# Optimization experiments

Hardware: AMD Instinct MI355X
Metric: run time of the kernel (lower is better)

The kernel has to match this reference:

```python
import jax, jax.numpy as jnp
import numpy as np

V, D, B, S, T, MAXLEN = 32000, 256, 4, 512, 256, 512


def _gru(x, Wih, Whh, bih, bhh):
    """torch-style GRU over x:[B,L,Din] -> [B,L,D]. Weight rows ordered [r,z,n]."""
    Dh = Whh.shape[1]
    xW = x @ Wih.T + bih  # [B,L,3D] precompute input projections

    def step(h, xw):
        hW = h @ Whh.T + bhh
        xr, xz, xn = jnp.split(xw, 3, axis=-1)
        hr, hz, hn = jnp.split(hW, 3, axis=-1)
        r = jax.nn.sigmoid(xr + hr)
        z = jax.nn.sigmoid(xz + hz)
        n = jnp.tanh(xn + r * hn)
        h = (1.0 - z) * n + z * h
        return h, h

    h0 = jnp.zeros((x.shape[0], Dh), x.dtype)
    _, ys = jax.lax.scan(step, h0, jnp.swapaxes(xW, 0, 1))
    return jnp.swapaxes(ys, 0, 1)


def setup_inputs() -> dict:
    key = jax.random.key(0)
    ks = jax.random.split(key, 24)

    def n(k, shape, scale=0.02):
        return (jax.random.normal(k, shape, jnp.float32) * scale).astype(jnp.float32)

    inp = {
        "src": jax.random.randint(ks[0], (B, S), 0, V),
        "tgt": jax.random.randint(ks[1], (B, T), 0, V),
        "emb": n(ks[2], (V, D)),
        "pos": n(ks[3], (MAXLEN, D)),
        # encoder forward direction
        "ef_wih": n(ks[4], (3 * D, D)), "ef_whh": n(ks[5], (3 * D, D)),
        "ef_bih": n(ks[6], (3 * D,)), "ef_bhh": n(ks[7], (3 * D,)),
        # encoder backward direction
        "eb_wih": n(ks[8], (3 * D, D)), "eb_whh": n(ks[9], (3 * D, D)),
        "eb_bih": n(ks[10], (3 * D,)), "eb_bhh": n(ks[11], (3 * D,)),
        # decoder
        "d_wih": n(ks[12], (3 * D, D)), "d_whh": n(ks[13], (3 * D, D)),
        "d_bih": n(ks[14], (3 * D,)), "d_bhh": n(ks[15], (3 * D,)),
        "Wq": n(ks[16], (D, D)),
        "Wk": n(ks[17], (D, 2 * D)),
        "Wgen": n(ks[18], (V, 3 * D)), "bgen": n(ks[19], (V,)),
        "Wgate": n(ks[20], (1, 3 * D)), "bgate": n(ks[21], (1,)),
    }
    return inp


def reference(src, tgt, emb, pos,
              ef_wih, ef_whh, ef_bih, ef_bhh,
              eb_wih, eb_whh, eb_bih, eb_bhh,
              d_wih, d_whh, d_bih, d_bhh,
              Wq, Wk, Wgen, bgen, Wgate, bgate):
    b, s = src.shape
    t = tgt.shape[1]
    d = emb.shape[1]
    v = emb.shape[0]

    src_emb = emb[src] + pos[:s][None]          # [B,S,D]
    enc_f = _gru(src_emb, ef_wih, ef_whh, ef_bih, ef_bhh)
    enc_b = _gru(src_emb[:, ::-1], eb_wih, eb_whh, eb_bih, eb_bhh)[:, ::-1]
    enc_out = jnp.concatenate([enc_f, enc_b], axis=-1)  # [B,S,2D]

    tgt_emb = emb[tgt] + pos[:t][None]
    dec_out = _gru(tgt_emb, d_wih, d_whh, d_bih, d_bhh)  # [B,T,D]

    Q = dec_out @ Wq.T                           # [B,T,D]
    K = enc_out @ Wk.T                           # [B,S,D]
    scores = jnp.einsum('btd,bsd->bts', Q, K) / jnp.sqrt(jnp.asarray(d, jnp.float32))
    pos_probs = jax.nn.softmax(scores, axis=-1)  # [B,T,S]

    # copy distribution: scatter attention mass into vocab buckets (== one_hot bmm)
    P_copy = jnp.zeros((b, t, v), pos_probs.dtype).at[
        jnp.arange(b)[:, None, None],
        jnp.arange(t)[None, :, None],
        src[:, None, :],
    ].add(pos_probs)

    ctx_f = jnp.einsum('bts,bsd->btd', pos_probs, enc_f)
    ctx_b = jnp.einsum('bts,bsd->btd', pos_probs, enc_b)
    combined = jnp.concatenate([dec_out, ctx_f, ctx_b], axis=-1)  # [B,T,3D]

    P_gen = jax.nn.softmax(combined @ Wgen.T + bgen, axis=-1)     # [B,T,V]
    gate = jax.nn.sigmoid(combined @ Wgate.T + bgate)             # [B,T,1]
    return gate * P_gen + (1.0 - gate) * P_copy
```

## Files before the change

kernel.cpp:

```cpp
#include <hip/hip_runtime.h>
#include <hip/hip_bf16.h>
#include <math.h>

#define VV   32000
#define DIM  256
#define BB   4
#define SS   512
#define TT   256
#define D2   512
#define D3   768

typedef __attribute__((ext_vector_type(8))) short s16x8;
typedef __attribute__((ext_vector_type(4))) float f32x4;

__device__ __forceinline__ float rcp_(float x) { return __builtin_amdgcn_rcpf(x); }
__device__ __forceinline__ float sigmoidf_(float x) { return rcp_(1.0f + __expf(-x)); }
__device__ __forceinline__ float tanhf_(float x) {
    float t = __expf(-2.0f * x);
    return (1.0f - t) * rcp_(1.0f + t);
}
__device__ __forceinline__ short f2bf(float f) {
    unsigned u = __float_as_uint(f);
    u += 0x7FFFu + ((u >> 16) & 1u);
    return (short)(u >> 16);
}

#define BAR_LGKM() asm volatile("s_waitcnt lgkmcnt(0)\n\ts_barrier" ::: "memory")

struct PDesc {
    const int* tok;
    const float* Wt;
    const float* bias;
    float* C;
    int M;
    int lmask;
};

__global__ __launch_bounds__(512) void k_proj(const float* __restrict__ emb,
                                              const float* __restrict__ pos,
                                              PDesc p0, PDesc p1, PDesc p2) {
    PDesc p = (blockIdx.z == 0) ? p0 : ((blockIdx.z == 1) ? p1 : p2);
    int brow = blockIdx.y * 256;
    if (brow >= p.M) return;
    int bcol = blockIdx.x * 128;

    __shared__ __align__(16) short As[256 * 32];
    __shared__ __align__(16) short Bs[128 * 32];
    int tid = threadIdx.x;
    int lane = tid & 63, wv = tid >> 6;
    int wm = wv >> 1, wn = wv & 1;
    const int ll = lane & 15, lh = lane >> 4;

    f32x4 acc[4][4];
#pragma unroll
    for (int i = 0; i < 4; i++)
#pragma unroll
        for (int j = 0; j < 4; j++) acc[i][j] = (f32x4){0.f, 0.f, 0.f, 0.f};

    const int ar = tid >> 1, ak = (tid & 1) * 16;
    const int br = tid >> 2, bk = (tid & 3) * 8;
    const int grow = brow + ar;
    const float* erow = emb + (size_t)p.tok[grow] * DIM;
    const float* prow = pos + (size_t)(grow & p.lmask) * DIM;

    for (int k0 = 0; k0 < DIM; k0 += 32) {
        float4 a0 = *(const float4*)(erow + k0 + ak);
        float4 a1 = *(const float4*)(erow + k0 + ak + 4);
        float4 a2 = *(const float4*)(erow + k0 + ak + 8);
        float4 a3 = *(const float4*)(erow + k0 + ak + 12);
        float4 q0 = *(const float4*)(prow + k0 + ak);
        float4 q1 = *(const float4*)(prow + k0 + ak + 4);
        float4 q2 = *(const float4*)(prow + k0 + ak + 8);
        float4 q3 = *(const float4*)(prow + k0 + ak + 12);
        const float* bp = &p.Wt[(size_t)(bcol + br) * DIM + k0 + bk];
        float4 b0 = *(const float4*)bp;
        float4 b1 = *(const float4*)(bp + 4);
        s16x8 va0, va1, vb;
        va0[0] = f2bf(a0.x + q0.x); va0[1] = f2bf(a0.y + q0.y);
        va0[2] = f2bf(a0.z + q0.z); va0[3] = f2bf(a0.w + q0.w);
        va0[4] = f2bf(a1.x + q1.x); va0[5] = f2bf(a1.y + q1.y);
        va0[6] = f2bf(a1.z + q1.z); va0[7] = f2bf(a1.w + q1.w);
        va1[0] = f2bf(a2.x + q2.x); va1[1] = f2bf(a2.y + q2.y);
        va1[2] = f2bf(a2.z + q2.z); va1[3] = f2bf(a2.w + q2.w);
        va1[4] = f2bf(a3.x + q3.x); va1[5] = f2bf(a3.y + q3.y);
        va1[6] = f2bf(a3.z + q3.z); va1[7] = f2bf(a3.w + q3.w);
        vb[0] = f2bf(b0.x); vb[1] = f2bf(b0.y); vb[2] = f2bf(b0.z); vb[3] = f2bf(b0.w);
        vb[4] = f2bf(b1.x); vb[5] = f2bf(b1.y); vb[6] = f2bf(b1.z); vb[7] = f2bf(b1.w);

        __syncthreads();
        *(s16x8*)&As[ar * 32 + ak] = va0;
        *(s16x8*)&As[ar * 32 + ak + 8] = va1;
        *(s16x8*)&Bs[br * 32 + bk] = vb;
        __syncthreads();

        s16x8 af[4], bf[4];
#pragma unroll
        for (int mt = 0; mt < 4; ++mt)
            af[mt] = *(const s16x8*)&As[(wm * 64 + mt * 16 + ll) * 32 + lh * 8];
#pragma unroll
        for (int nt = 0; nt < 4; ++nt)
            bf[nt] = *(const s16x8*)&Bs[(wn * 64 + nt * 16 + ll) * 32 + lh * 8];
#pragma unroll
        for (int mt = 0; mt < 4; ++mt)
#pragma unroll
            for (int nt = 0; nt < 4; ++nt)
                acc[mt][nt] = __builtin_amdgcn_mfma_f32_16x16x32_bf16(af[mt], bf[nt], acc[mt][nt], 0, 0, 0);
    }

#pragma unroll
    for (int mt = 0; mt < 4; ++mt) {
        int row = brow + wm * 64 + mt * 16 + lh * 4;
#pragma unroll
        for (int nt = 0; nt < 4; ++nt) {
            int col = bcol + wn * 64 + nt * 16 + ll;
            float bv = p.bias[col];
#pragma unroll
            for (int q = 0; q < 4; ++q)
                p.C[(size_t)(row + q) * D3 + col] = acc[mt][nt][q] + bv;
        }
    }
}

struct GDesc {
    const float* A; int lda;
    const float* Bt; int ldb;
    const float* bias;
    float* C; int ldc;
    int M, N;
};

#define BMM 128
#define BNN 128
#define BKK 8

__global__ __launch_bounds__(256) void k_gemmb(GDesc d0, GDesc d1, GDesc d2) {
    GDesc d = (blockIdx.z == 0) ? d0 : ((blockIdx.z == 1) ? d1 : d2);
    int brow = blockIdx.y * BMM, bcol = blockIdx.x * BNN;
    if (brow >= d.M || bcol >= d.N) return;

    __shared__ float As[BKK][BMM + 4];
    __shared__ float Bs[BKK][BNN + 4];
    const int K = d.lda;
    int tid = threadIdx.x;
    int tx = tid & 15, ty = tid >> 4;
    float acc[8][8];
#pragma unroll
    for (int i = 0; i < 8; i++)
#pragma unroll
        for (int j = 0; j < 8; j++) acc[i][j] = 0.0f;

    int lr = tid >> 1;
    int lk = (tid & 1) * 4;
    for (int k0 = 0; k0 < K; k0 += BKK) {
        float4 a4 = *(const float4*)&d.A[(size_t)(brow + lr) * d.lda + k0 + lk];
        float4 b4 = *(const float4*)&d.Bt[(size_t)(bcol + lr) * d.ldb + k0 + lk];
        As[lk + 0][lr] = a4.x; As[lk + 1][lr] = a4.y; As[lk + 2][lr] = a4.z; As[lk + 3][lr] = a4.w;
        Bs[lk + 0][lr] = b4.x; Bs[lk + 1][lr] = b4.y; Bs[lk + 2][lr] = b4.z; Bs[lk + 3][lr] = b4.w;
        __syncthreads();
#pragma unroll
        for (int kk = 0; kk < BKK; kk++) {
            float4 a0 = *(const float4*)&As[kk][ty * 8];
            float4 a1 = *(const float4*)&As[kk][ty * 8 + 4];
            float4 b0 = *(const float4*)&Bs[kk][tx * 8];
            float4 b1 = *(const float4*)&Bs[kk][tx * 8 + 4];
            float av[8] = {a0.x, a0.y, a0.z, a0.w, a1.x, a1.y, a1.z, a1.w};
            float bv[8] = {b0.x, b0.y, b0.z, b0.w, b1.x, b1.y, b1.z, b1.w};
#pragma unroll
            for (int i = 0; i < 8; i++)
#pragma unroll
                for (int j = 0; j < 8; j++) acc[i][j] += av[i] * bv[j];
        }
        __syncthreads();
    }

#pragma unroll
    for (int i = 0; i < 8; i++) {
        size_t row = brow + ty * 8 + i;
        float4 c0 = make_float4(acc[i][0], acc[i][1], acc[i][2], acc[i][3]);
        float4 c1 = make_float4(acc[i][4], acc[i][5], acc[i][6], acc[i][7]);
        *(float4*)&d.C[row * d.ldc + bcol + tx * 8] = c0;
        *(float4*)&d.C[row * d.ldc + bcol + tx * 8 + 4] = c1;
    }
}

#define HSTRIDE 576
#define HBUF    (4 * HSTRIDE)
#define NCVT8   ((size_t)VV * D3 / 8)

__global__ __launch_bounds__(1024) void k_gru(const float* __restrict__ ef_x,
                                              const float* __restrict__ eb_x,
                                              const float* __restrict__ d_x,
                                              const float* __restrict__ ef_whh, const float* __restrict__ ef_bhh,
                                              const float* __restrict__ eb_whh, const float* __restrict__ eb_bhh,
                                              const float* __restrict__ d_whh, const float* __restrict__ d_bhh,
                                              float* __restrict__ enc_out,
                                              float* __restrict__ dec_out,
                                              const float* __restrict__ wgen,
                                              short* __restrict__ wgen_bf,
                                              float* __restrict__ rowsum,
                                              int do_cvt) {
    int tid = threadIdx.x;
    int bid = blockIdx.x;

    if (bid >= 3) {
        int cb = bid - 3;
        if (cb == 0) rowsum[tid] = 0.0f;
        if (do_cvt) {
            size_t i = (size_t)cb * 1024 + tid;
            if (i < NCVT8) {
                const float4* p = (const float4*)(wgen + i * 8);
                float4 a = p[0], b4 = p[1];
                s16x8 v;
                v[0] = f2bf(a.x); v[1] = f2bf(a.y); v[2] = f2bf(a.z); v[3] = f2bf(a.w);
                v[4] = f2bf(b4.x); v[5] = f2bf(b4.y); v[6] = f2bf(b4.z); v[7] = f2bf(b4.w);
                *(s16x8*)(wgen_bf + i * 8) = v;
            }
        }
        return;
    }

    __shared__ __align__(16) char hb[2 * HBUF];
    int dir = bid;
    const float *xw, *Whh, *bhh;
    int L;
    if (dir == 0)      { xw = ef_x; Whh = ef_whh; bhh = ef_bhh; L = SS; }
    else if (dir == 1) { xw = eb_x; Whh = eb_whh; bhh = eb_bhh; L = SS; }
    else               { xw = d_x;  Whh = d_whh;  bhh = d_bhh;  L = TT; }

    const int wv = tid >> 6;
    const int lane = tid & 63;
    const int jj = lane & 15;
    const int hi = lane >> 4;
    const int b = hi;

    if (tid < 288) {
        f32x4 z = {0.f, 0.f, 0.f, 0.f};
        *(f32x4*)(hb + tid * 16) = z;
    }

    s16x8 wf[3][8];
#pragma unroll
    for (int g = 0; g < 3; ++g) {
        const int nrow = g * 256 + wv * 16 + jj;
        const float* wp = Whh + (size_t)nrow * 256 + hi * 8;
#pragma unroll
        for (int sk = 0; sk < 8; ++sk) {
            float4 w0 = *(const float4*)(wp + sk * 32);
            float4 w1 = *(const float4*)(wp + sk * 32 + 4);
            s16x8 v;
            v[0] = f2bf(w0.x); v[1] = f2bf(w0.y); v[2] = f2bf(w0.z); v[3] = f2bf(w0.w);
            v[4] = f2bf(w1.x); v[5] = f2bf(w1.y); v[6] = f2bf(w1.z); v[7] = f2bf(w1.w);
            wf[g][sk] = v;
        }
    }

    const int j0 = wv * 16 + jj;
    const float br0 = bhh[j0], bz0 = bhh[256 + j0], bn0 = bhh[512 + j0];

    const int arow = jj >> 2;
    const int abase = arow * HSTRIDE + hi * 16;
    const int wo0 = b * HSTRIDE + 2 * j0;

    const int s0 = (dir == 1) ? (L - 1) : 0;
    const int sst = (dir == 1) ? -1 : 1;
    const float* xq = xw + ((size_t)b * L + s0) * D3 + j0;
    float* op;
    int ostride;
    if (dir == 2) { op = dec_out + ((size_t)b * TT + s0) * DIM + j0; ostride = sst * DIM; }
    else          { op = enc_out + ((size_t)b * SS + s0) * D2 + (dir == 1 ? DIM : 0) + j0; ostride = sst * D2; }
    const int xstride = sst * D3;

    float c0 = xq[0], c1 = xq[256], c2 = xq[512];

    float h0 = 0.f;
    int cur = 0;
    __syncthreads();

    for (int st = 0; st < L; ++st) {
        xq += xstride;
        float n0 = xq[0], n1 = xq[256], n2 = xq[512];

        const char* hcur = hb + cur * HBUF;
        f32x4 a00 = {0.f, 0.f, 0.f, 0.f}, a10 = a00, a20 = a00;
#pragma unroll
        for (int sk = 0; sk < 8; ++sk) {
            s16x8 af = *(const s16x8*)(hcur + abase + 64 * sk);
            a00 = __builtin_amdgcn_mfma_f32_16x16x32_bf16(af, wf[0][sk], a00, 0, 0, 0);
            a10 = __builtin_amdgcn_mfma_f32_16x16x32_bf16(af, wf[1][sk], a10, 0, 0, 0);
            a20 = __builtin_amdgcn_mfma_f32_16x16x32_bf16(af, wf[2][sk], a20, 0, 0, 0);
        }

        float r0 = sigmoidf_(c0 + a00[0] + br0);
        float z0 = sigmoidf_(c1 + a10[0] + bz0);
        float nn0 = tanhf_(c2 + r0 * (a20[0] + bn0));
        h0 = (1.f - z0) * nn0 + z0 * h0;

        char* hnxt = hb + (cur ^ 1) * HBUF;
        *(short*)(hnxt + wo0) = f2bf(h0);
        op[0] = h0;
        BAR_LGKM();

        cur ^= 1;
        c0 = n0; c1 = n1; c2 = n2;
        op += ostride;
    }
}

__global__ __launch_bounds__(512) void k_attn(const float* __restrict__ Qb,
                                              const float* __restrict__ Kb,
                                              const float* __restrict__ enc_out,
                                              const float* __restrict__ dec_out,
                                              const float* __restrict__ Wgate,
                                              const float* __restrict__ bgate,
                                              float* __restrict__ probs,
                                              short* __restrict__ cmb,
                                              float* __restrict__ gate) {
    __shared__ float q[DIM];
    __shared__ float sc[SS];
    __shared__ float red[512];
    __shared__ float par[2][2][DIM];
    int row = blockIdx.x;
    int b = row >> 8;
    int tid = threadIdx.x;

    if (tid < DIM) q[tid] = Qb[(size_t)row * DIM + tid];
    __syncthreads();

    const float scale = 0.0625f;
    {
        const float* kr = Kb + ((size_t)b * SS + tid) * DIM;
        float acc = 0.0f;
        for (int k = 0; k < DIM; k += 4) {
            float4 k4 = *(const float4*)&kr[k];
            acc += k4.x * q[k] + k4.y * q[k + 1] + k4.z * q[k + 2] + k4.w * q[k + 3];
        }
        sc[tid] = acc * scale;
    }
    __syncthreads();

    red[tid] = sc[tid];
    __syncthreads();
    for (int o = 256; o > 0; o >>= 1) {
        if (tid < o) red[tid] = fmaxf(red[tid], red[tid + o]);
        __syncthreads();
    }
    float m = red[0];
    __syncthreads();

    float e0 = __expf(sc[tid] - m);
    sc[tid] = e0;
    red[tid] = e0;
    __syncthreads();
    for (int o = 256; o > 0; o >>= 1) {
        if (tid < o) red[tid] += red[tid + o];
        __syncthreads();
    }
    float inv = rcp_(red[0]);
    __syncthreads();

    sc[tid] *= inv;
    probs[(size_t)row * SS + tid] = sc[tid];
    __syncthreads();

    {
        int d = tid & 255, sh = tid >> 8;
        float accf = 0.0f, accb = 0.0f;
        const float* ep = enc_out + ((size_t)b * SS + sh * 256) * D2 + d;
        const float* pp = &sc[sh * 256];
        for (int s = 0; s < 256; s++) {
            float p = pp[s];
            accf += p * ep[(size_t)s * D2];
            accb += p * ep[(size_t)s * D2 + DIM];
        }
        par[sh][0][d] = accf;
        par[sh][1][d] = accb;
    }
    __syncthreads();

    if (tid < DIM) {
        float af = par[0][0][tid] + par[1][0][tid];
        float ab = par[0][1][tid] + par[1][1][tid];
        float dv = dec_out[(size_t)row * DIM + tid];
        cmb[(size_t)row * D3 + tid] = f2bf(dv);
        cmb[(size_t)row * D3 + DIM + tid] = f2bf(af);
        cmb[(size_t)row * D3 + 2 * DIM + tid] = f2bf(ab);
        red[tid] = dv * Wgate[tid] + af * Wgate[DIM + tid] + ab * Wgate[2 * DIM + tid];
    }
    __syncthreads();
    for (int o = 128; o > 0; o >>= 1) {
        if (tid < o) red[tid] += red[tid + o];
        __syncthreads();
    }
    if (tid == 0) gate[row] = sigmoidf_(red[0] + bgate[0]);
}

__global__ __launch_bounds__(512) void k_gen_bf(const short* __restrict__ A,
                                                const short* __restrict__ Bbf,
                                                const float* __restrict__ bias,
                                                float* __restrict__ C,
                                                float* __restrict__ rowsum) {
    __shared__ __align__(16) short As[256 * 32];
    __shared__ __align__(16) short Bs[128 * 32];
    int tid = threadIdx.x;
    int lane = tid & 63, wv = tid >> 6;
    int wm = wv >> 1, wn = wv & 1;
    int brow = blockIdx.y * 256, bcol = blockIdx.x * 128;
    f32x4 acc[4][4];
#pragma unroll
    for (int i = 0; i < 4; i++)
#pragma unroll
        for (int j = 0; j < 4; j++) acc[i][j] = (f32x4){0.f, 0.f, 0.f, 0.f};

    const int ca0 = tid, ca1 = tid + 512, cb = tid;
    const int ll = lane & 15, lh = lane >> 4;

    for (int k0 = 0; k0 < D3; k0 += 32) {
        s16x8 va0 = *(const s16x8*)&A[(size_t)(brow + (ca0 >> 2)) * D3 + k0 + (ca0 & 3) * 8];
        s16x8 va1 = *(const s16x8*)&A[(size_t)(brow + (ca1 >> 2)) * D3 + k0 + (ca1 & 3) * 8];
        s16x8 vb  = *(const s16x8*)&Bbf[(size_t)(bcol + (cb >> 2)) * D3 + k0 + (cb & 3) * 8];

        __syncthreads();
        *(s16x8*)&As[ca0 * 8] = va0;
        *(s16x8*)&As[ca1 * 8] = va1;
        *(s16x8*)&Bs[cb * 8] = vb;
        __syncthreads();

        s16x8 af[4], bf[4];
#pragma unroll
        for (int mt = 0; mt < 4; ++mt)
            af[mt] = *(const s16x8*)&As[(wm * 64 + mt * 16 + ll) * 32 + lh * 8];
#pragma unroll
        for (int nt = 0; nt < 4; ++nt)
            bf[nt] = *(const s16x8*)&Bs[(wn * 64 + nt * 16 + ll) * 32 + lh * 8];
#pragma unroll
        for (int mt = 0; mt < 4; ++mt)
#pragma unroll
            for (int nt = 0; nt < 4; ++nt)
                acc[mt][nt] = __builtin_amdgcn_mfma_f32_16x16x32_bf16(af[mt], bf[nt], acc[mt][nt], 0, 0, 0);
    }

#pragma unroll
    for (int nt = 0; nt < 4; ++nt) {
        float bv = bias[bcol + wn * 64 + nt * 16 + ll];
#pragma unroll
        for (int mt = 0; mt < 4; ++mt)
#pragma unroll
            for (int q = 0; q < 4; ++q) acc[mt][nt][q] += bv;
    }

#pragma unroll
    for (int mt = 0; mt < 4; ++mt) {
        int row = brow + wm * 64 + mt * 16 + lh * 4;
#pragma unroll
        for (int nt = 0; nt < 4; ++nt) {
            int col = bcol + wn * 64 + nt * 16 + ll;
#pragma unroll
            for (int q = 0; q < 4; ++q)
                C[(size_t)(row + q) * VV + col] = acc[mt][nt][q];
        }
    }

#pragma unroll
    for (int mt = 0; mt < 4; ++mt) {
#pragma unroll
        for (int q = 0; q < 4; ++q) {
            float se = __expf(acc[mt][0][q]) + __expf(acc[mt][1][q]) +
                       __expf(acc[mt][2][q]) + __expf(acc[mt][3][q]);
#pragma unroll
            for (int off = 1; off < 16; off <<= 1)
                se += __shfl_xor(se, off);
            if (ll == 0) {
                int row = brow + wm * 64 + mt * 16 + lh * 4 + q;
                atomicAdd(&rowsum[row], se);
            }
        }
    }
}

__global__ __launch_bounds__(512) void k_gen(const short* __restrict__ A,
                                             const float* __restrict__ Bw,
                                             const float* __restrict__ bias,
                                             float* __restrict__ C,
                                             float* __restrict__ rowsum) {
    __shared__ __align__(16) short As[256 * 32];
    __shared__ __align__(16) short Bs[128 * 32];
    int tid = threadIdx.x;
    int lane = tid & 63, wv = tid >> 6;
    int wm = wv >> 1, wn = wv & 1;
    int brow = blockIdx.y * 256, bcol = blockIdx.x * 128;
    f32x4 acc[4][4];
#pragma unroll
    for (int i = 0; i < 4; i++)
#pragma unroll
        for (int j = 0; j < 4; j++) acc[i][j] = (f32x4){0.f, 0.f, 0.f, 0.f};

    const int ca0 = tid, ca1 = tid + 512, cb = tid;
    const int ll = lane & 15, lh = lane >> 4;

    for (int k0 = 0; k0 < D3; k0 += 32) {
        s16x8 va0 = *(const s16x8*)&A[(size_t)(brow + (ca0 >> 2)) * D3 + k0 + (ca0 & 3) * 8];
        s16x8 va1 = *(const s16x8*)&A[(size_t)(brow + (ca1 >> 2)) * D3 + k0 + (ca1 & 3) * 8];
        const float* bp = &Bw[(size_t)(bcol + (cb >> 2)) * D3 + k0 + (cb & 3) * 8];
        float4 b0 = *(const float4*)bp;
        float4 b1 = *(const float4*)(bp + 4);
        s16x8 vb;
        vb[0] = f2bf(b0.x); vb[1] = f2bf(b0.y); vb[2] = f2bf(b0.z); vb[3] = f2bf(b0.w);
        vb[4] = f2bf(b1.x); vb[5] = f2bf(b1.y); vb[6] = f2bf(b1.z); vb[7] = f2bf(b1.w);

        __syncthreads();
        *(s16x8*)&As[ca0 * 8] = va0;
        *(s16x8*)&As[ca1 * 8] = va1;
        *(s16x8*)&Bs[cb * 8] = vb;
        __syncthreads();

        s16x8 af[4], bf[4];
#pragma unroll
        for (int mt = 0; mt < 4; ++mt)
            af[mt] = *(const s16x8*)&As[(wm * 64 + mt * 16 + ll) * 32 + lh * 8];
#pragma unroll
        for (int nt = 0; nt < 4; ++nt)
            bf[nt] = *(const s16x8*)&Bs[(wn * 64 + nt * 16 + ll) * 32 + lh * 8];
#pragma unroll
        for (int mt = 0; mt < 4; ++mt)
#pragma unroll
            for (int nt = 0; nt < 4; ++nt)
                acc[mt][nt] = __builtin_amdgcn_mfma_f32_16x16x32_bf16(af[mt], bf[nt], acc[mt][nt], 0, 0, 0);
    }

#pragma unroll
    for (int nt = 0; nt < 4; ++nt) {
        float bv = bias[bcol + wn * 64 + nt * 16 + ll];
#pragma unroll
        for (int mt = 0; mt < 4; ++mt)
#pragma unroll
            for (int q = 0; q < 4; ++q) acc[mt][nt][q] += bv;
    }

#pragma unroll
    for (int mt = 0; mt < 4; ++mt) {
        int row = brow + wm * 64 + mt * 16 + lh * 4;
#pragma unroll
        for (int nt = 0; nt < 4; ++nt) {
            int col = bcol + wn * 64 + nt * 16 + ll;
#pragma unroll
            for (int q = 0; q < 4; ++q)
                C[(size_t)(row + q) * VV + col] = acc[mt][nt][q];
        }
    }

#pragma unroll
    for (int mt = 0; mt < 4; ++mt) {
#pragma unroll
        for (int q = 0; q < 4; ++q) {
            float se = __expf(acc[mt][0][q]) + __expf(acc[mt][1][q]) +
                       __expf(acc[mt][2][q]) + __expf(acc[mt][3][q]);
#pragma unroll
            for (int off = 1; off < 16; off <<= 1)
                se += __shfl_xor(se, off);
            if (ll == 0) {
                int row = brow + wm * 64 + mt * 16 + lh * 4 + q;
                atomicAdd(&rowsum[row], se);
            }
        }
    }
}

__global__ __launch_bounds__(256) void k_finsc(const int* __restrict__ src,
                                               const float* __restrict__ probs,
                                               const float* __restrict__ gate,
                                               const float* __restrict__ rowsum,
                                               float* __restrict__ out) {
    int row = blockIdx.x;
    int b = row >> 8;
    int tid = threadIdx.x;
    float g = gate[row];
    float inv = g / rowsum[row];
    float* op = out + (size_t)row * VV;

    for (int i = tid; i < VV / 4; i += 256) {
        float4 l = *(const float4*)&op[i * 4];
        l.x = __expf(l.x) * inv;
        l.y = __expf(l.y) * inv;
        l.z = __expf(l.z) * inv;
        l.w = __expf(l.w) * inv;
        *(float4*)&op[i * 4] = l;
    }
    __syncthreads();

    float og = 1.0f - g;
#pragma unroll
    for (int h = 0; h < 2; ++h) {
        int s = tid + h * 256;
        float val = og * probs[(size_t)row * SS + s];
        atomicAdd(&op[src[b * SS + s]], val);
    }
}

extern "C" void kernel_launch(void* const* d_in, const int* in_sizes, int n_in,
                              void* d_out, int out_size, void* d_ws, size_t ws_size,
                              hipStream_t stream) {
    const int*   src    = (const int*)d_in[0];
    const int*   tgt    = (const int*)d_in[1];
    const float* emb    = (const float*)d_in[2];
    const float* pos    = (const float*)d_in[3];
    const float* ef_wih = (const float*)d_in[4];
    const float* ef_whh = (const float*)d_in[5];
    const float* ef_bih = (const float*)d_in[6];
    const float* ef_bhh = (const float*)d_in[7];
    const float* eb_wih = (const float*)d_in[8];
    const float* eb_whh = (const float*)d_in[9];
    const float* eb_bih = (const float*)d_in[10];
    const float* eb_bhh = (const float*)d_in[11];
    const float* d_wih  = (const float*)d_in[12];
    const float* d_whh  = (const float*)d_in[13];
    const float* d_bih  = (const float*)d_in[14];
    const float* d_bhh  = (const float*)d_in[15];
    const float* Wq     = (const float*)d_in[16];
    const float* Wk     = (const float*)d_in[17];
    const float* Wgen   = (const float*)d_in[18];
    const float* bgen   = (const float*)d_in[19];
    const float* Wgate  = (const float*)d_in[20];
    const float* bgate  = (const float*)d_in[21];
    float* out = (float*)d_out;
    float* ws  = (float*)d_ws;

    float* ef_x     = ws;
    float* eb_x     = ef_x + (size_t)BB * SS * D3;
    float* d_x      = eb_x + (size_t)BB * SS * D3;
    float* enc_out  = d_x + (size_t)BB * TT * D3;
    float* dec_out  = enc_out + (size_t)BB * SS * D2;
    float* Qb       = dec_out + (size_t)BB * TT * DIM;
    float* Kb       = Qb + (size_t)BB * TT * DIM;
    float* probs    = Kb + (size_t)BB * SS * DIM;
    short* cmb_bf   = (short*)(probs + (size_t)BB * TT * SS);
    float* gate     = (float*)(cmb_bf + (size_t)BB * TT * D3);
    float* rowsum   = gate + 1024;
    short* wgen_bf  = (short*)(rowsum + 1024);
    const bool use_bf = ws_size >= (size_t)((char*)(wgen_bf + (size_t)VV * D3) - (char*)d_ws);

    {
        PDesc e0 = {src, ef_wih, ef_bih, ef_x, BB * SS, SS - 1};
        PDesc e1 = {src, eb_wih, eb_bih, eb_x, BB * SS, SS - 1};
        PDesc e2 = {tgt, d_wih, d_bih, d_x, BB * TT, TT - 1};
        k_proj<<<dim3(D3 / 128, BB * SS / 256, 3), 512, 0, stream>>>(emb, pos, e0, e1, e2);
    }

    {
        int ncvtb = (int)((NCVT8 + 1023) / 1024);
        k_gru<<<3 + ncvtb, 1024, 0, stream>>>(ef_x, eb_x, d_x,
                                              ef_whh, ef_bhh, eb_whh, eb_bhh, d_whh, d_bhh,
                                              enc_out, dec_out,
                                              Wgen, wgen_bf, rowsum, use_bf ? 1 : 0);
    }

    {
        GDesc q0 = {dec_out, DIM, Wq, DIM, nullptr, Qb, DIM, BB * TT, DIM};
        GDesc q1 = {enc_out, D2, Wk, D2, nullptr, Kb, DIM, BB * SS, DIM};
        k_gemmb<<<dim3(DIM / BNN, BB * SS / BMM, 2), 256, 0, stream>>>(q0, q1, q1);
    }

    k_attn<<<BB * TT, 512, 0, stream>>>(Qb, Kb, enc_out, dec_out, Wgate, bgate,
                                        probs, cmb_bf, gate);

    if (use_bf)
        k_gen_bf<<<dim3(VV / 128, (BB * TT) / 256), 512, 0, stream>>>(cmb_bf, wgen_bf, bgen, out, rowsum);
    else
        k_gen<<<dim3(VV / 128, (BB * TT) / 256), 512, 0, stream>>>(cmb_bf, Wgen, bgen, out, rowsum);

    k_finsc<<<BB * TT, 256, 0, stream>>>(src, probs, gate, rowsum, out);
}
```

Baseline: 1.072 ms.

## Rework GRU to 512 threads, MFMA Q/K projection, bf16 logits intermediate

The GRU kernel now runs 512 threads per block, with each wave computing two 16-column slices. The gate math switches to exact-division sigmoid and tanh. The fp32 FMA GEMM for the Q/K projections is replaced with a bf16 MFMA tile kernel. When the workspace is large enough, generator logits are stored as bf16 in a separate buffer and expanded by a new finisher kernel, which halves the intermediate logit traffic at the cost of logit precision. Exact division may lengthen the serial recurrence step.

```diff
diff --git a/kernel.cpp b/kernel.cpp
--- a/kernel.cpp
+++ b/kernel.cpp
@@ -15,14 +15,18 @@
 
 __device__ __forceinline__ float rcp_(float x) { return __builtin_amdgcn_rcpf(x); }
 __device__ __forceinline__ float sigmoidf_(float x) { return rcp_(1.0f + __expf(-x)); }
-__device__ __forceinline__ float tanhf_(float x) {
-    float t = __expf(-2.0f * x);
-    return (1.0f - t) * rcp_(1.0f + t);
+__device__ __forceinline__ float sigmoid_p(float x) { return 1.0f / (1.0f + __expf(-x)); }
+__device__ __forceinline__ float tanh_p(float x) {
+    float e2 = __expf(2.0f * x);
+    return (e2 - 1.0f) / (e2 + 1.0f);
 }
 __device__ __forceinline__ short f2bf(float f) {
     unsigned u = __float_as_uint(f);
     u += 0x7FFFu + ((u >> 16) & 1u);
     return (short)(u >> 16);
+}
+__device__ __forceinline__ float bf2f(short s) {
+    return __uint_as_float(((unsigned)(unsigned short)s) << 16);
 }
 
 #define BAR_LGKM() asm volatile("s_waitcnt lgkmcnt(0)\n\ts_barrier" ::: "memory")
@@ -121,65 +125,83 @@
     }
 }
 
-struct GDesc {
-    const float* A; int lda;
-    const float* Bt; int ldb;
-    const float* bias;
-    float* C; int ldc;
-    int M, N;
+struct QDesc {
+    const float* A; int K;
+    const float* Bt;
+    float* C;
+    int M;
 };
 
-#define BMM 128
-#define BNN 128
-#define BKK 8
-
-__global__ __launch_bounds__(256) void k_gemmb(GDesc d0, GDesc d1, GDesc d2) {
-    GDesc d = (blockIdx.z == 0) ? d0 : ((blockIdx.z == 1) ? d1 : d2);
-    int brow = blockIdx.y * BMM, bcol = blockIdx.x * BNN;
-    if (brow >= d.M || bcol >= d.N) return;
-
-    __shared__ float As[BKK][BMM + 4];
-    __shared__ float Bs[BKK][BNN + 4];
-    const int K = d.lda;
+__global__ __launch_bounds__(512) void k_qk(QDesc q0d, QDesc q1d) {
+    QDesc p = (blockIdx.z == 0) ? q0d : q1d;
+    int brow = blockIdx.y * 256;
+    if (brow >= p.M) return;
+    int bcol = blockIdx.x * 128;
+    const int K = p.K;
+
+    __shared__ __align__(16) short As[256 * 32];
+    __shared__ __align__(16) short Bs[128 * 32];
     int tid = threadIdx.x;
-    int tx = tid & 15, ty = tid >> 4;
-    float acc[8][8];
-#pragma unroll
-    for (int i = 0; i < 8; i++)
-#pragma unroll
-        for (int j = 0; j < 8; j++) acc[i][j] = 0.0f;
-
-    int lr = tid >> 1;
-    int lk = (tid & 1) * 4;
-    for (int k0 = 0; k0 < K; k0 += BKK) {
-        float4 a4 = *(const float4*)&d.A[(size_t)(brow + lr) * d.lda + k0 + lk];
-        float4 b4 = *(const float4*)&d.Bt[(size_t)(bcol + lr) * d.ldb + k0 + lk];
-        As[lk + 0][lr] = a4.x; As[lk + 1][lr] = a4.y; As[lk + 2][lr] = a4.z; As[lk + 3][lr] = a4.w;
-        Bs[lk + 0][lr] = b4.x; Bs[lk + 1][lr] = b4.y; Bs[lk + 2][lr] = b4.z; Bs[lk + 3][lr] = b4.w;
+    int lane = tid & 63, wv = tid >> 6;
+    int wm = wv >> 1, wn = wv & 1;
+    const int ll = lane & 15, lh = lane >> 4;
+
+    f32x4 acc[4][4];
+#pragma unroll
+    for (int i = 0; i < 4; i++)
+#pragma unroll
+        for (int j = 0; j < 4; j++) acc[i][j] = (f32x4){0.f, 0.f, 0.f, 0.f};
+
+    const int ar = tid >> 1, ak = (tid & 1) * 16;
+    const int br = tid >> 2, bk = (tid & 3) * 8;
+
+    for (int k0 = 0; k0 < K; k0 += 32) {
+        const float* ap = &p.A[(size_t)(brow + ar) * K + k0 + ak];
+        float4 a0 = *(const float4*)ap;
+        float4 a1 = *(const float4*)(ap + 4);
+        float4 a2 = *(const float4*)(ap + 8);
+        float4 a3 = *(const float4*)(ap + 12);
+        const float* bp = &p.Bt[(size_t)(bcol + br) * K + k0 + bk];
+        float4 b0 = *(const float4*)bp;
+        float4 b1 = *(const float4*)(bp + 4);
+        s16x8 va0, va1, vb;
+        va0[0] = f2bf(a0.x); va0[1] = f2bf(a0.y); va0[2] = f2bf(a0.z); va0[3] = f2bf(a0.w);
+        va0[4] = f2bf(a1.x); va0[5] = f2bf(a1.y); va0[6] = f2bf(a1.z); va0[7] = f2bf(a1.w);
+        va1[0] = f2bf(a2.x); va1[1] = f2bf(a2.y); va1[2] = f2bf(a2.z); va1[3] = f2bf(a2.w);
+        va1[4] = f2bf(a3.x); va1[5] = f2bf(a3.y); va1[6] = f2bf(a3.z); va1[7] = f2bf(a3.w);
+        vb[0] = f2bf(b0.x); vb[1] = f2bf(b0.y); vb[2] = f2bf(b0.z); vb[3] = f2bf(b0.w);
+        vb[4] = f2bf(b1.x); vb[5] = f2bf(b1.y); vb[6] = f2bf(b1.z); vb[7] = f2bf(b1.w);
+
         __syncthreads();
-#pragma unroll
-        for (int kk = 0; kk < BKK; kk++) {
-            float4 a0 = *(const float4*)&As[kk][ty * 8];
-            float4 a1 = *(const float4*)&As[kk][ty * 8 + 4];
-            float4 b0 = *(const float4*)&Bs[kk][tx * 8];
-            float4 b1 = *(const float4*)&Bs[kk][tx * 8 + 4];
-            float av[8] = {a0.x, a0.y, a0.z, a0.w, a1.x, a1.y, a1.z, a1.w};
-            float bv[8] = {b0.x, b0.y, b0.z, b0.w, b1.x, b1.y, b1.z, b1.w};
-#pragma unroll
-            for (int i = 0; i < 8; i++)
-#pragma unroll
-                for (int j = 0; j < 8; j++) acc[i][j] += av[i] * bv[j];
-        }
+        *(s16x8*)&As[ar * 32 + ak] = va0;
+        *(s16x8*)&As[ar * 32 + ak + 8] = va1;
+        *(s16x8*)&Bs[br * 32 + bk] = vb;
         __syncthreads();
-    }
-
-#pragma unroll
-    for (int i = 0; i < 8; i++) {
-        size_t row = brow + ty * 8 + i;
-        float4 c0 = make_float4(acc[i][0], acc[i][1], acc[i][2], acc[i][3]);
-        float4 c1 = make_float4(acc[i][4], acc[i][5], acc[i][6], acc[i][7]);
-        *(float4*)&d.C[row * d.ldc + bcol + tx * 8] = c0;
-        *(float4*)&d.C[row * d.ldc + bcol + tx * 8 + 4] = c1;
+
+        s16x8 af[4], bf[4];
+#pragma unroll
+        for (int mt = 0; mt < 4; ++mt)
+            af[mt] = *(const s16x8*)&As[(wm * 64 + mt * 16 + ll) * 32 + lh * 8];
+#pragma unroll
+        for (int nt = 0; nt < 4; ++nt)
+            bf[nt] = *(const s16x8*)&Bs[(wn * 64 + nt * 16 + ll) * 32 + lh * 8];
+#pragma unroll
+        for (int mt = 0; mt < 4; ++mt)
+#pragma unroll
+            for (int nt = 0; nt < 4; ++nt)
+                acc[mt][nt] = __builtin_amdgcn_mfma_f32_16x16x32_bf16(af[mt], bf[nt], acc[mt][nt], 0, 0, 0);
+    }
+
+#pragma unroll
+    for (int mt = 0; mt < 4; ++mt) {
+        int row = brow + wm * 64 + mt * 16 + lh * 4;
+#pragma unroll
+        for (int nt = 0; nt < 4; ++nt) {
+            int col = bcol + wn * 64 + nt * 16 + ll;
+#pragma unroll
+            for (int q = 0; q < 4; ++q)
+                p.C[(size_t)(row + q) * DIM + col] = acc[mt][nt][q];
+        }
     }
 }
 
@@ -187,26 +209,26 @@
 #define HBUF    (4 * HSTRIDE)
 #define NCVT8   ((size_t)VV * D3 / 8)
 
-__global__ __launch_bounds__(1024) void k_gru(const float* __restrict__ ef_x,
-                                              const float* __restrict__ eb_x,
-                                              const float* __restrict__ d_x,
-                                              const float* __restrict__ ef_whh, const float* __restrict__ ef_bhh,
-                                              const float* __restrict__ eb_whh, const float* __restrict__ eb_bhh,
-                                              const float* __restrict__ d_whh, const float* __restrict__ d_bhh,
-                                              float* __restrict__ enc_out,
-                                              float* __restrict__ dec_out,
-                                              const float* __restrict__ wgen,
-                                              short* __restrict__ wgen_bf,
-                                              float* __restrict__ rowsum,
-                                              int do_cvt) {
+__global__ __launch_bounds__(512, 2) void k_gru(const float* __restrict__ ef_x,
+                                                const float* __restrict__ eb_x,
+                                                const float* __restrict__ d_x,
+                                                const float* __restrict__ ef_whh, const float* __restrict__ ef_bhh,
+                                                const float* __restrict__ eb_whh, const float* __restrict__ eb_bhh,
+                                                const float* __restrict__ d_whh, const float* __restrict__ d_bhh,
+                                                float* __restrict__ enc_out,
+                                                float* __restrict__ dec_out,
+                                                const float* __restrict__ wgen,
+                                                short* __restrict__ wgen_bf,
+                                                float* __restrict__ rowsum,
+                                                int do_cvt) {
     int tid = threadIdx.x;
     int bid = blockIdx.x;
 
     if (bid >= 3) {
         int cb = bid - 3;
-        if (cb == 0) rowsum[tid] = 0.0f;
+        if (cb == 0) { rowsum[tid] = 0.0f; rowsum[tid + 512] = 0.0f; }
         if (do_cvt) {
-            size_t i = (size_t)cb * 1024 + tid;
+            size_t i = (size_t)cb * 512 + tid;
             if (i < NCVT8) {
                 const float4* p = (const float4*)(wgen + i * 8);
                 float4 a = p[0], b4 = p[1];
@@ -238,28 +260,32 @@
         *(f32x4*)(hb + tid * 16) = z;
     }
 
-    s16x8 wf[3][8];
-#pragma unroll
-    for (int g = 0; g < 3; ++g) {
-        const int nrow = g * 256 + wv * 16 + jj;
-        const float* wp = Whh + (size_t)nrow * 256 + hi * 8;
-#pragma unroll
-        for (int sk = 0; sk < 8; ++sk) {
-            float4 w0 = *(const float4*)(wp + sk * 32);
-            float4 w1 = *(const float4*)(wp + sk * 32 + 4);
-            s16x8 v;
-            v[0] = f2bf(w0.x); v[1] = f2bf(w0.y); v[2] = f2bf(w0.z); v[3] = f2bf(w0.w);
-            v[4] = f2bf(w1.x); v[5] = f2bf(w1.y); v[6] = f2bf(w1.z); v[7] = f2bf(w1.w);
-            wf[g][sk] = v;
-        }
-    }
-
-    const int j0 = wv * 16 + jj;
+    s16x8 wf[3][2][8];
+#pragma unroll
+    for (int g = 0; g < 3; ++g)
+#pragma unroll
+        for (int t = 0; t < 2; ++t) {
+            const int nrow = g * 256 + wv * 32 + t * 16 + jj;
+            const float* wp = Whh + (size_t)nrow * 256 + hi * 8;
+#pragma unroll
+            for (int sk = 0; sk < 8; ++sk) {
+                float4 w0 = *(const float4*)(wp + sk * 32);
+                float4 w1 = *(const float4*)(wp + sk * 32 + 4);
+                s16x8 v;
+                v[0] = f2bf(w0.x); v[1] = f2bf(w0.y); v[2] = f2bf(w0.z); v[3] = f2bf(w0.w);
+                v[4] = f2bf(w1.x); v[5] = f2bf(w1.y); v[6] = f2bf(w1.z); v[7] = f2bf(w1.w);
+                wf[g][t][sk] = v;
+            }
+        }
+
+    const int j0 = wv * 32 + jj, j1 = j0 + 16;
     const float br0 = bhh[j0], bz0 = bhh[256 + j0], bn0 = bhh[512 + j0];
+    const float br1 = bhh[j1], bz1 = bhh[256 + j1], bn1 = bhh[512 + j1];
 
     const int arow = jj >> 2;
     const int abase = arow * HSTRIDE + hi * 16;
     const int wo0 = b * HSTRIDE + 2 * j0;
+    const int wo1 = b * HSTRIDE + 2 * j1;
 
     const int s0 = (dir == 1) ? (L - 1) : 0;
     const int sst = (dir == 1) ? -1 : 1;
@@ -270,38 +296,47 @@
     else          { op = enc_out + ((size_t)b * SS + s0) * D2 + (dir == 1 ? DIM : 0) + j0; ostride = sst * D2; }
     const int xstride = sst * D3;
 
-    float c0 = xq[0], c1 = xq[256], c2 = xq[512];
-
-    float h0 = 0.f;
+    float c0 = xq[0], c1 = xq[256], c2 = xq[512], c3 = xq[16], c4 = xq[272], c5 = xq[528];
+
+    float h0 = 0.f, h1 = 0.f;
     int cur = 0;
     __syncthreads();
 
     for (int st = 0; st < L; ++st) {
         xq += xstride;
-        float n0 = xq[0], n1 = xq[256], n2 = xq[512];
+        float n0 = xq[0], n1 = xq[256], n2 = xq[512], n3 = xq[16], n4 = xq[272], n5 = xq[528];
 
         const char* hcur = hb + cur * HBUF;
-        f32x4 a00 = {0.f, 0.f, 0.f, 0.f}, a10 = a00, a20 = a00;
+        f32x4 a00 = {0.f, 0.f, 0.f, 0.f}, a01 = a00, a10 = a00, a11 = a00, a20 = a00, a21 = a00;
 #pragma unroll
         for (int sk = 0; sk < 8; ++sk) {
             s16x8 af = *(const s16x8*)(hcur + abase + 64 * sk);
-            a00 = __builtin_amdgcn_mfma_f32_16x16x32_bf16(af, wf[0][sk], a00, 0, 0, 0);
-            a10 = __builtin_amdgcn_mfma_f32_16x16x32_bf16(af, wf[1][sk], a10, 0, 0, 0);
-            a20 = __builtin_amdgcn_mfma_f32_16x16x32_bf16(af, wf[2][sk], a20, 0, 0, 0);
-        }
-
-        float r0 = sigmoidf_(c0 + a00[0] + br0);
-        float z0 = sigmoidf_(c1 + a10[0] + bz0);
-        float nn0 = tanhf_(c2 + r0 * (a20[0] + bn0));
+            a00 = __builtin_amdgcn_mfma_f32_16x16x32_bf16(af, wf[0][0][sk], a00, 0, 0, 0);
+            a01 = __builtin_amdgcn_mfma_f32_16x16x32_bf16(af, wf[0][1][sk], a01, 0, 0, 0);
+            a10 = __builtin_amdgcn_mfma_f32_16x16x32_bf16(af, wf[1][0][sk], a10, 0, 0, 0);
+            a11 = __builtin_amdgcn_mfma_f32_16x16x32_bf16(af, wf[1][1][sk], a11, 0, 0, 0);
+            a20 = __builtin_amdgcn_mfma_f32_16x16x32_bf16(af, wf[2][0][sk], a20, 0, 0, 0);
+            a21 = __builtin_amdgcn_mfma_f32_16x16x32_bf16(af, wf[2][1][sk], a21, 0, 0, 0);
+        }
+
+        float r0 = sigmoid_p(c0 + a00[0] + br0);
+        float z0 = sigmoid_p(c1 + a10[0] + bz0);
+        float nn0 = tanh_p(c2 + r0 * (a20[0] + bn0));
         h0 = (1.f - z0) * nn0 + z0 * h0;
+        float r1 = sigmoid_p(c3 + a01[0] + br1);
+        float z1 = sigmoid_p(c4 + a11[0] + bz1);
+        float nn1 = tanh_p(c5 + r1 * (a21[0] + bn1));
+        h1 = (1.f - z1) * nn1 + z1 * h1;
 
         char* hnxt = hb + (cur ^ 1) * HBUF;
         *(short*)(hnxt + wo0) = f2bf(h0);
+        *(short*)(hnxt + wo1) = f2bf(h1);
         op[0] = h0;
+        op[16] = h1;
         BAR_LGKM();
 
         cur ^= 1;
-        c0 = n0; c1 = n1; c2 = n2;
+        c0 = n0; c1 = n1; c2 = n2; c3 = n3; c4 = n4; c5 = n5;
         op += ostride;
     }
 }
@@ -394,51 +429,94 @@
     if (tid == 0) gate[row] = sigmoidf_(red[0] + bgate[0]);
 }
 
+#define GEN_PROLOGUE()                                                      \
+    __shared__ __align__(16) short As[256 * 32];                            \
+    __shared__ __align__(16) short Bs[128 * 32];                            \
+    int tid = threadIdx.x;                                                  \
+    int lane = tid & 63, wv = tid >> 6;                                     \
+    int wm = wv >> 1, wn = wv & 1;                                          \
+    int brow = blockIdx.y * 256, bcol = blockIdx.x * 128;                   \
+    f32x4 acc[4][4];                                                        \
+    _Pragma("unroll") for (int i = 0; i < 4; i++)                           \
+        _Pragma("unroll") for (int j = 0; j < 4; j++)                       \
+            acc[i][j] = (f32x4){0.f, 0.f, 0.f, 0.f};                        \
+    const int ca0 = tid, ca1 = tid + 512, cb = tid;                         \
+    const int ll = lane & 15, lh = lane >> 4;
+
+#define GEN_MAINLOOP(LOAD_B)                                                \
+    for (int k0 = 0; k0 < D3; k0 += 32) {                                   \
+        s16x8 va0 = *(const s16x8*)&A[(size_t)(brow + (ca0 >> 2)) * D3 + k0 + (ca0 & 3) * 8]; \
+        s16x8 va1 = *(const s16x8*)&A[(size_t)(brow + (ca1 >> 2)) * D3 + k0 + (ca1 & 3) * 8]; \
+        s16x8 vb; LOAD_B;                                                   \
+        __syncthreads();                                                    \
+        *(s16x8*)&As[ca0 * 8] = va0;                                        \
+        *(s16x8*)&As[ca1 * 8] = va1;                                        \
+        *(s16x8*)&Bs[cb * 8] = vb;                                          \
+        __syncthreads();                                                    \
+        s16x8 af[4], bf[4];                                                 \
+        _Pragma("unroll") for (int mt = 0; mt < 4; ++mt)                    \
+            af[mt] = *(const s16x8*)&As[(wm * 64 + mt * 16 + ll) * 32 + lh * 8]; \
+        _Pragma("unroll") for (int nt = 0; nt < 4; ++nt)                    \
+            bf[nt] = *(const s16x8*)&Bs[(wn * 64 + nt * 16 + ll) * 32 + lh * 8]; \
+        _Pragma("unroll") for (int mt = 0; mt < 4; ++mt)                    \
+            _Pragma("unroll") for (int nt = 0; nt < 4; ++nt)                \
+                acc[mt][nt] = __builtin_amdgcn_mfma_f32_16x16x32_bf16(af[mt], bf[nt], acc[mt][nt], 0, 0, 0); \
+    }
+
+#define LOADB_BF  vb = *(const s16x8*)&Bbf[(size_t)(bcol + (cb >> 2)) * D3 + k0 + (cb & 3) * 8]
+#define LOADB_F32 do {                                                      \
+        const float* bp = &Bw[(size_t)(bcol + (cb >> 2)) * D3 + k0 + (cb & 3) * 8]; \
+        float4 b0 = *(const float4*)bp; float4 b1 = *(const float4*)(bp + 4); \
+        vb[0] = f2bf(b0.x); vb[1] = f2bf(b0.y); vb[2] = f2bf(b0.z); vb[3] = f2bf(b0.w); \
+        vb[4] = f2bf(b1.x); vb[5] = f2bf(b1.y); vb[6] = f2bf(b1.z); vb[7] = f2bf(b1.w); } while (0)
+
+#define GEN_ROWSUM(EXPR)                                                    \
+    _Pragma("unroll") for (int mt = 0; mt < 4; ++mt)                        \
+        _Pragma("unroll") for (int q = 0; q < 4; ++q) {                     \
+            float se = (EXPR);                                              \
+            _Pragma("unroll") for (int off = 1; off < 16; off <<= 1)        \
+                se += __shfl_xor(se, off);                                  \
+            if (ll == 0) atomicAdd(&rowsum[brow + wm * 64 + mt * 16 + lh * 4 + q], se); \
+        }
+
+__global__ __launch_bounds__(512) void k_genb(const short* __restrict__ A,
+                                              const short* __restrict__ Bbf,
+                                              const float* __restrict__ bias,
+                                              short* __restrict__ C16,
+                                              float* __restrict__ rowsum) {
+    GEN_PROLOGUE();
+    GEN_MAINLOOP(LOADB_BF);
+    short lr[4][4][4];
+#pragma unroll
+    for (int nt = 0; nt < 4; ++nt) {
+        float bv = bias[bcol + wn * 64 + nt * 16 + ll];
+#pragma unroll
+        for (int mt = 0; mt < 4; ++mt)
+#pragma unroll
+            for (int q = 0; q < 4; ++q) lr[mt][nt][q] = f2bf(acc[mt][nt][q] + bv);
+    }
+#pragma unroll
+    for (int mt = 0; mt < 4; ++mt) {
+        int row = brow + wm * 64 + mt * 16 + lh * 4;
+#pragma unroll
+        for (int nt = 0; nt < 4; ++nt) {
+            int col = bcol + wn * 64 + nt * 16 + ll;
+#pragma unroll
+            for (int q = 0; q < 4; ++q)
+                C16[(size_t)(row + q) * VV + col] = lr[mt][nt][q];
+        }
+    }
+    GEN_ROWSUM(__expf(bf2f(lr[mt][0][q])) + __expf(bf2f(lr[mt][1][q])) +
+               __expf(bf2f(lr[mt][2][q])) + __expf(bf2f(lr[mt][3][q])));
+}
+
 __global__ __launch_bounds__(512) void k_gen_bf(const short* __restrict__ A,
                                                 const short* __restrict__ Bbf,
                                                 const float* __restrict__ bias,
                                                 float* __restrict__ C,
                                                 float* __restrict__ rowsum) {
-    __shared__ __align__(16) short As[256 * 32];
-    __shared__ __align__(16) short Bs[128 * 32];
-    int tid = threadIdx.x;
-    int lane = tid & 63, wv = tid >> 6;
-    int wm = wv >> 1, wn = wv & 1;
-    int brow = blockIdx.y * 256, bcol = blockIdx.x * 128;
-    f32x4 acc[4][4];
-#pragma unroll
-    for (int i = 0; i < 4; i++)
-#pragma unroll
-        for (int j = 0; j < 4; j++) acc[i][j] = (f32x4){0.f, 0.f, 0.f, 0.f};
-
-    const int ca0 = tid, ca1 = tid + 512, cb = tid;
-    const int ll = lane & 15, lh = lane >> 4;
-
-    for (int k0 = 0; k0 < D3; k0 += 32) {
-        s16x8 va0 = *(const s16x8*)&A[(size_t)(brow + (ca0 >> 2)) * D3 + k0 + (ca0 & 3) * 8];
-        s16x8 va1 = *(const s16x8*)&A[(size_t)(brow + (ca1 >> 2)) * D3 + k0 + (ca1 & 3) * 8];
-        s16x8 vb  = *(const s16x8*)&Bbf[(size_t)(bcol + (cb >> 2)) * D3 + k0 + (cb & 3) * 8];
-
-        __syncthreads();
-        *(s16x8*)&As[ca0 * 8] = va0;
-        *(s16x8*)&As[ca1 * 8] = va1;
-        *(s16x8*)&Bs[cb * 8] = vb;
-        __syncthreads();
-
-        s16x8 af[4], bf[4];
-#pragma unroll
-        for (int mt = 0; mt < 4; ++mt)
-            af[mt] = *(const s16x8*)&As[(wm * 64 + mt * 16 + ll) * 32 + lh * 8];
-#pragma unroll
-        for (int nt = 0; nt < 4; ++nt)
-            bf[nt] = *(const s16x8*)&Bs[(wn * 64 + nt * 16 + ll) * 32 + lh * 8];
-#pragma unroll
-        for (int mt = 0; mt < 4; ++mt)
-#pragma unroll
-            for (int nt = 0; nt < 4; ++nt)
-                acc[mt][nt] = __builtin_amdgcn_mfma_f32_16x16x32_bf16(af[mt], bf[nt], acc[mt][nt], 0, 0, 0);
-    }
-
+    GEN_PROLOGUE();
+    GEN_MAINLOOP(LOADB_BF);
 #pragma unroll
     for (int nt = 0; nt < 4; ++nt) {
         float bv = bias[bcol + wn * 64 + nt * 16 + ll];
@@ -447,7 +525,6 @@
 #pragma unroll
             for (int q = 0; q < 4; ++q) acc[mt][nt][q] += bv;
     }
-
 #pragma unroll
     for (int mt = 0; mt < 4; ++mt) {
         int row = brow + wm * 64 + mt * 16 + lh * 4;
@@ -459,22 +536,8 @@
                 C[(size_t)(row + q) * VV + col] = acc[mt][nt][q];
         }
     }
-
-#pragma unroll
-    for (int mt = 0; mt < 4; ++mt) {
-#pragma unroll
-        for (int q = 0; q < 4; ++q) {
-            float se = __expf(acc[mt][0][q]) + __expf(acc[mt][1][q]) +
-                       __expf(acc[mt][2][q]) + __expf(acc[mt][3][q]);
-#pragma unroll
-            for (int off = 1; off < 16; off <<= 1)
-                se += __shfl_xor(se, off);
-            if (ll == 0) {
-                int row = brow + wm * 64 + mt * 16 + lh * 4 + q;
-                atomicAdd(&rowsum[row], se);
-            }
-        }
-    }
+    GEN_ROWSUM(__expf(acc[mt][0][q]) + __expf(acc[mt][1][q]) +
+               __expf(acc[mt][2][q]) + __expf(acc[mt][3][q]));
 }
 
 __global__ __launch_bounds__(512) void k_gen(const short* __restrict__ A,
@@ -482,51 +545,8 @@
                                              const float* __restrict__ bias,
                                              float* __restrict__ C,
                                              float* __restrict__ rowsum) {
-    __shared__ __align__(16) short As[256 * 32];
-    __shared__ __align__(16) short Bs[128 * 32];
-    int tid = threadIdx.x;
-    int lane = tid & 63, wv = tid >> 6;
-    int wm = wv >> 1, wn = wv & 1;
-    int brow = blockIdx.y * 256, bcol = blockIdx.x * 128;
-    f32x4 acc[4][4];
-#pragma unroll
-    for (int i = 0; i < 4; i++)
-#pragma unroll
-        for (int j = 0; j < 4; j++) acc[i][j] = (f32x4){0.f, 0.f, 0.f, 0.f};
-
-    const int ca0 = tid, ca1 = tid + 512, cb = tid;
-    const int ll = lane & 15, lh = lane >> 4;
-
-    for (int k0 = 0; k0 < D3; k0 += 32) {
-        s16x8 va0 = *(const s16x8*)&A[(size_t)(brow + (ca0 >> 2)) * D3 + k0 + (ca0 & 3) * 8];
-        s16x8 va1 = *(const s16x8*)&A[(size_t)(brow + (ca1 >> 2)) * D3 + k0 + (ca1 & 3) * 8];
-        const float* bp = &Bw[(size_t)(bcol + (cb >> 2)) * D3 + k0 + (cb & 3) * 8];
-        float4 b0 = *(const float4*)bp;
-        float4 b1 = *(const float4*)(bp + 4);
-        s16x8 vb;
-        vb[0] = f2bf(b0.x); vb[1] = f2bf(b0.y); vb[2] = f2bf(b0.z); vb[3] = f2bf(b0.w);
-        vb[4] = f2bf(b1.x); vb[5] = f2bf(b1.y); vb[6] = f2bf(b1.z); vb[7] = f2bf(b1.w);
-
-        __syncthreads();
-        *(s16x8*)&As[ca0 * 8] = va0;
-        *(s16x8*)&As[ca1 * 8] = va1;
-        *(s16x8*)&Bs[cb * 8] = vb;
-        __syncthreads();
-
-        s16x8 af[4], bf[4];
-#pragma unroll
-        for (int mt = 0; mt < 4; ++mt)
-            af[mt] = *(const s16x8*)&As[(wm * 64 + mt * 16 + ll) * 32 + lh * 8];
-#pragma unroll
-        for (int nt = 0; nt < 4; ++nt)
-            bf[nt] = *(const s16x8*)&Bs[(wn * 64 + nt * 16 + ll) * 32 + lh * 8];
-#pragma unroll
-        for (int mt = 0; mt < 4; ++mt)
-#pragma unroll
-            for (int nt = 0; nt < 4; ++nt)
-                acc[mt][nt] = __builtin_amdgcn_mfma_f32_16x16x32_bf16(af[mt], bf[nt], acc[mt][nt], 0, 0, 0);
-    }
-
+    GEN_PROLOGUE();
+    GEN_MAINLOOP(LOADB_F32);
 #pragma unroll
     for (int nt = 0; nt < 4; ++nt) {
         float bv = bias[bcol + wn * 64 + nt * 16 + ll];
@@ -535,7 +555,6 @@
 #pragma unroll
             for (int q = 0; q < 4; ++q) acc[mt][nt][q] += bv;
     }
-
 #pragma unroll
     for (int mt = 0; mt < 4; ++mt) {
         int row = brow + wm * 64 + mt * 16 + lh * 4;
@@ -547,21 +566,42 @@
                 C[(size_t)(row + q) * VV + col] = acc[mt][nt][q];
         }
     }
-
-#pragma unroll
-    for (int mt = 0; mt < 4; ++mt) {
-#pragma unroll
-        for (int q = 0; q < 4; ++q) {
-            float se = __expf(acc[mt][0][q]) + __expf(acc[mt][1][q]) +
-                       __expf(acc[mt][2][q]) + __expf(acc[mt][3][q]);
-#pragma unroll
-            for (int off = 1; off < 16; off <<= 1)
-                se += __shfl_xor(se, off);
-            if (ll == 0) {
-                int row = brow + wm * 64 + mt * 16 + lh * 4 + q;
-                atomicAdd(&rowsum[row], se);
-            }
-        }
+    GEN_ROWSUM(__expf(acc[mt][0][q]) + __expf(acc[mt][1][q]) +
+               __expf(acc[mt][2][q]) + __expf(acc[mt][3][q]));
+}
+
+__global__ __launch_bounds__(256) void k_finsc_bf(const int* __restrict__ src,
+                                                  const float* __restrict__ probs,
+                                                  const float* __restrict__ gate,
+                                                  const float* __restrict__ rowsum,
+                                                  const short* __restrict__ L16,
+                                                  float* __restrict__ out) {
+    int row = blockIdx.x;
+    int b = row >> 8;
+    int tid = threadIdx.x;
+    float g = gate[row];
+    float inv = g / rowsum[row];
+    const short* lp = L16 + (size_t)row * VV;
+    float* op = out + (size_t)row * VV;
+
+    for (int i = tid; i < VV / 8; i += 256) {
+        s16x8 l8 = *(const s16x8*)&lp[i * 8];
+        float4 o0, o1;
+        o0.x = __expf(bf2f(l8[0])) * inv; o0.y = __expf(bf2f(l8[1])) * inv;
+        o0.z = __expf(bf2f(l8[2])) * inv; o0.w = __expf(bf2f(l8[3])) * inv;
+        o1.x = __expf(bf2f(l8[4])) * inv; o1.y = __expf(bf2f(l8[5])) * inv;
+        o1.z = __expf(bf2f(l8[6])) * inv; o1.w = __expf(bf2f(l8[7])) * inv;
+        *(float4*)&op[i * 8] = o0;
+        *(float4*)&op[i * 8 + 4] = o1;
+    }
+    __syncthreads();
+
+    float og = 1.0f - g;
+#pragma unroll
+    for (int h = 0; h < 2; ++h) {
+        int s = tid + h * 256;
+        float val = og * probs[(size_t)row * SS + s];
+        atomicAdd(&op[src[b * SS + s]], val);
     }
 }
 
@@ -636,7 +676,9 @@
     float* gate     = (float*)(cmb_bf + (size_t)BB * TT * D3);
     float* rowsum   = gate + 1024;
     short* wgen_bf  = (short*)(rowsum + 1024);
-    const bool use_bf = ws_size >= (size_t)((char*)(wgen_bf + (size_t)VV * D3) - (char*)d_ws);
+    short* logit_bf = wgen_bf + (size_t)VV * D3;
+    const bool use_bf  = ws_size >= (size_t)((char*)(wgen_bf + (size_t)VV * D3) - (char*)d_ws);
+    const bool use_lbf = ws_size >= (size_t)((char*)(logit_bf + (size_t)VV * BB * TT) - (char*)d_ws);
 
     {
         PDesc e0 = {src, ef_wih, ef_bih, ef_x, BB * SS, SS - 1};
@@ -646,26 +688,31 @@
     }
 
     {
-        int ncvtb = (int)((NCVT8 + 1023) / 1024);
-        k_gru<<<3 + ncvtb, 1024, 0, stream>>>(ef_x, eb_x, d_x,
-                                              ef_whh, ef_bhh, eb_whh, eb_bhh, d_whh, d_bhh,
-                                              enc_out, dec_out,
-                                              Wgen, wgen_bf, rowsum, use_bf ? 1 : 0);
+        int ncvtb = (int)((NCVT8 + 511) / 512);
+        k_gru<<<3 + ncvtb, 512, 0, stream>>>(ef_x, eb_x, d_x,
+                                             ef_whh, ef_bhh, eb_whh, eb_bhh, d_whh, d_bhh,
+                                             enc_out, dec_out,
+                                             Wgen, wgen_bf, rowsum, use_bf ? 1 : 0);
     }
 
     {
-        GDesc q0 = {dec_out, DIM, Wq, DIM, nullptr, Qb, DIM, BB * TT, DIM};
-        GDesc q1 = {enc_out, D2, Wk, D2, nullptr, Kb, DIM, BB * SS, DIM};
-        k_gemmb<<<dim3(DIM / BNN, BB * SS / BMM, 2), 256, 0, stream>>>(q0, q1, q1);
+        QDesc q0 = {dec_out, DIM, Wq, Qb, BB * TT};
+        QDesc q1 = {enc_out, D2, Wk, Kb, BB * SS};
+        k_qk<<<dim3(DIM / 128, BB * SS / 256, 2), 512, 0, stream>>>(q0, q1);
     }
 
     k_attn<<<BB * TT, 512, 0, stream>>>(Qb, Kb, enc_out, dec_out, Wgate, bgate,
                                         probs, cmb_bf, gate);
 
-    if (use_bf)
-        k_gen_bf<<<dim3(VV / 128, (BB * TT) / 256), 512, 0, stream>>>(cmb_bf, wgen_bf, bgen, out, rowsum);
-    else
-        k_gen<<<dim3(VV / 128, (BB * TT) / 256), 512, 0, stream>>>(cmb_bf, Wgen, bgen, out, rowsum);
-
-    k_finsc<<<BB * TT, 256, 0, stream>>>(src, probs, gate, rowsum, out);
-}
+    dim3 gg(VV / 128, (BB * TT) / 256);
+    if (use_lbf) {
+        k_genb<<<gg, 512, 0, stream>>>(cmb_bf, wgen_bf, bgen, logit_bf, rowsum);
+        k_finsc_bf<<<BB * TT, 256, 0, stream>>>(src, probs, gate, rowsum, logit_bf, out);
+    } else if (use_bf) {
+        k_gen_bf<<<gg, 512, 0, stream>>>(cmb_bf, wgen_bf, bgen, out, rowsum);
+        k_finsc<<<BB * TT, 256, 0, stream>>>(src, probs, gate, rowsum, out);
+    } else {
+        k_gen<<<gg, 512, 0, stream>>>(cmb_bf, Wgen, bgen, out, rowsum);
+        k_finsc<<<BB * TT, 256, 0, stream>>>(src, probs, gate, rowsum, out);
+    }
+}
```

New measurement: 1.074 ms. Within noise of the previous version (+0.2%).
